# Kernel optimization log

Hardware: AMD Instinct MI355X
Metric: run time of the kernel (lower is better)

## Reference

```python
import jax, jax.numpy as jnp
import numpy as np

N_HEAD, D_EMB, D_MLP, D_HEAD = 12, 768, 3072, 64
LN_EPS = 1e-5


def setup_inputs() -> dict:
    key = jax.random.key(0)
    ks = jax.random.split(key, 12)
    s = 0.02
    return {
        "x": jax.random.normal(ks[0], (2, 4096, D_EMB), dtype=jnp.float32),
        "ln1_g": jnp.ones((D_EMB,), jnp.float32),
        "ln1_b": jnp.zeros((D_EMB,), jnp.float32),
        "wqkv_w": jax.random.normal(ks[1], (D_EMB, 3 * D_EMB), jnp.float32) * s,
        "wo_w": jax.random.normal(ks[2], (D_EMB, D_EMB), jnp.float32) * s,
        "wo_b": jnp.zeros((D_EMB,), jnp.float32),
        "ln2_g": jnp.ones((D_EMB,), jnp.float32),
        "ln2_b": jnp.zeros((D_EMB,), jnp.float32),
        "w1_w": jax.random.normal(ks[3], (D_EMB, D_MLP), jnp.float32) * s,
        "w1_b": jnp.zeros((D_MLP,), jnp.float32),
        "w2_w": jax.random.normal(ks[4], (D_MLP, D_EMB), jnp.float32) * s,
        "w2_b": jnp.zeros((D_EMB,), jnp.float32),
    }


def _layernorm(x, g, b):
    mu = jnp.mean(x, axis=-1, keepdims=True)
    var = jnp.var(x, axis=-1, keepdims=True)
    return (x - mu) * jax.lax.rsqrt(var + LN_EPS) * g + b


def _attn(x, wqkv_w, wo_w, wo_b):
    B, T, d = x.shape
    qkv = x @ wqkv_w  # [B,T,3d]
    q, k, v = jnp.split(qkv, 3, axis=-1)
    q = q.reshape(B, T, N_HEAD, D_HEAD).transpose(0, 2, 1, 3)  # [B,H,T,dh]
    k = k.reshape(B, T, N_HEAD, D_HEAD).transpose(0, 2, 1, 3)
    v = v.reshape(B, T, N_HEAD, D_HEAD).transpose(0, 2, 1, 3)
    A = jnp.einsum('bhqd,bhkd->bhqk', q, k) / np.sqrt(D_HEAD).astype(np.float32)
    mask = jnp.tril(jnp.ones((T, T), dtype=bool))
    A = jnp.where(mask, A, -jnp.inf)
    A = jax.nn.softmax(A - jax.lax.stop_gradient(jnp.max(A, axis=-1, keepdims=True)), axis=-1)
    y = jnp.einsum('bhqk,bhkd->bhqd', A, v)  # [B,H,T,dh]
    y = y.transpose(0, 2, 1, 3).reshape(B, T, d)
    return y @ wo_w + wo_b


def _mlp(x, w1_w, w1_b, w2_w, w2_b):
    h = jax.nn.gelu(x @ w1_w + w1_b, approximate=False)
    return h @ w2_w + w2_b


def reference(x, ln1_g, ln1_b, wqkv_w, wo_w, wo_b, ln2_g, ln2_b, w1_w, w1_b, w2_w, w2_b):
    x = x + _attn(_layernorm(x, ln1_g, ln1_b), wqkv_w, wo_w, wo_b)
    x = x + _mlp(_layernorm(x, ln2_g, ln2_b), w1_w, w1_b, w2_w, w2_b)
    return x
```

## Files before the change

### kernel.cpp

```cpp
#include <hip/hip_runtime.h>

#define T_SEQ 4096
#define D_EMB 768
#define N_HEAD 12
#define D_HEAD 64
#define D_MLP 3072
#define NTOK 8192
#define QSCALE 0.18033688011112043f

typedef __bf16 v8bf __attribute__((ext_vector_type(8)));
typedef float v4f __attribute__((ext_vector_type(4)));

template <int N> struct IC { static constexpr int value = N; };

__device__ __forceinline__ unsigned short f2bf(float f) {
    unsigned int u = __float_as_uint(f);
    unsigned int r = (u + 0x7fffu + ((u >> 16) & 1u)) >> 16;
    return (unsigned short)r;
}

__device__ __forceinline__ void g2lds16(const void* g, void* l) {
    __builtin_amdgcn_global_load_lds(
        (const __attribute__((address_space(1))) void*)g,
        (__attribute__((address_space(3))) void*)l, 16, 0, 0);
}

__device__ __forceinline__ int sg(int r) { return (r ^ (r >> 2)) & 3; }

__global__ void tcast_kernel(const float* __restrict__ in, unsigned short* __restrict__ out,
                             int K, int N) {
    __shared__ float tile[32][33];
    int k0 = blockIdx.y * 32, n0 = blockIdx.x * 32;
    int tx = threadIdx.x, ty = threadIdx.y;
    for (int i = ty; i < 32; i += 8)
        tile[i][tx] = in[(size_t)(k0 + i) * N + n0 + tx];
    __syncthreads();
    for (int i = ty; i < 32; i += 8)
        out[(size_t)(n0 + i) * K + k0 + tx] = f2bf(tile[tx][i]);
}

__global__ void vtrans_kernel(const unsigned short* __restrict__ in,
                              unsigned short* __restrict__ out) {
    __shared__ unsigned short tile[32][33];
    size_t base = (size_t)blockIdx.z * T_SEQ * D_HEAD;
    int t0 = blockIdx.x * 32, d0 = blockIdx.y * 32;
    int tx = threadIdx.x, ty = threadIdx.y;
    for (int i = ty; i < 32; i += 8)
        tile[i][tx] = in[base + (size_t)(t0 + i) * D_HEAD + d0 + tx];
    __syncthreads();
    size_t tbase = base + (size_t)(t0 >> 6) * 4096 + (t0 & 32);
    for (int i = ty; i < 32; i += 8)
        out[tbase + (size_t)(d0 + i) * 64 + tx] = tile[tx][i];
}

__global__ __launch_bounds__(256) void ln_kernel(const float* __restrict__ x,
                                                 const float* __restrict__ g,
                                                 const float* __restrict__ bta,
                                                 unsigned short* __restrict__ out) {
    int row = blockIdx.x;
    const float* xr = x + (size_t)row * D_EMB;
    int tid = threadIdx.x;
    float v[3];
    float s = 0.f, s2 = 0.f;
#pragma unroll
    for (int i = 0; i < 3; i++) {
        v[i] = xr[tid + i * 256];
        s += v[i];
        s2 += v[i] * v[i];
    }
#pragma unroll
    for (int o = 1; o < 64; o <<= 1) {
        s += __shfl_xor(s, o);
        s2 += __shfl_xor(s2, o);
    }
    __shared__ float red[8];
    int wave = tid >> 6, lane = tid & 63;
    if (lane == 0) { red[wave] = s; red[wave + 4] = s2; }
    __syncthreads();
    s = red[0] + red[1] + red[2] + red[3];
    s2 = red[4] + red[5] + red[6] + red[7];
    float mu = s * (1.f / 768.f);
    float var = s2 * (1.f / 768.f) - mu * mu;
    float rstd = rsqrtf(var + 1e-5f);
#pragma unroll
    for (int i = 0; i < 3; i++) {
        int c = tid + i * 256;
        out[(size_t)row * D_EMB + c] = f2bf((v[i] - mu) * rstd * g[c] + bta[c]);
    }
}

template <int EPI, int MT>
__global__ __launch_bounds__(256) void gemm_kernel(
    const unsigned short* __restrict__ A, const unsigned short* __restrict__ Bt, int K,
    int Nt, const float* __restrict__ bias, const float* __restrict__ resid,
    float* __restrict__ outF, unsigned short* __restrict__ outB,
    unsigned short* __restrict__ Qb, unsigned short* __restrict__ Kb,
    unsigned short* __restrict__ Vb) {
    constexpr int NAI = (MT == 128) ? 4 : 2;
    __shared__ unsigned short As[2][MT * 32];
    __shared__ unsigned short Bs[2][4096];
    const int tid = threadIdx.x;
    const int wave = tid >> 6, lane = tid & 63;
    const int n16 = lane & 15, kq = lane >> 4;
    const int moff = (wave >> 1) * (MT / 2), noff = (wave & 1) * 64;
    const int id = blockIdx.x;
    const int xcd = id & 7, s = id >> 3;
    const int mt = xcd * (NTOK / MT / 8) + s / Nt, nt_ = s % Nt;
    const long m0 = (long)mt * MT, nb0 = (long)nt_ * 128;

    const int c0 = (wave * 2 + 0) * 64 + lane;
    const int c1 = (wave * 2 + 1) * 64 + lane;
    const int r0 = c0 >> 2, r1 = c1 >> 2;
    const unsigned short* bP0 = Bt + (nb0 + r0) * K + (((c0 & 3) ^ sg(r0)) << 3);
    const unsigned short* bP1 = Bt + (nb0 + r1) * K + (((c1 & 3) ^ sg(r1)) << 3);
    const int ca = (MT == 128) ? c0 : (wave * 64 + lane);
    const int ra = ca >> 2;
    const unsigned short* aP0 = A + (m0 + ra) * K + (((ca & 3) ^ sg(ra)) << 3);
    const unsigned short* aP1 = (MT == 128)
        ? A + (m0 + r1) * K + (((c1 & 3) ^ sg(r1)) << 3) : nullptr;
    const int sn = sg(n16);
    const int fw = (noff + n16) * 32 + ((kq ^ sn) << 3);
    const int fa = (moff + n16) * 32 + ((kq ^ sn) << 3);

    const v4f vzero = {0.f, 0.f, 0.f, 0.f};
    v4f acc[4][NAI];
#pragma unroll
    for (int wi = 0; wi < 4; wi++)
#pragma unroll
        for (int ai = 0; ai < NAI; ai++) acc[wi][ai] = vzero;

    auto stage = [&](auto BUFC, int kpos) {
        constexpr int nb = decltype(BUFC)::value;
        if (MT == 128) {
            g2lds16(aP0 + kpos, &As[nb][(wave * 2 + 0) * 512]);
            g2lds16(aP1 + kpos, &As[nb][(wave * 2 + 1) * 512]);
        } else {
            g2lds16(aP0 + kpos, &As[nb][wave * 512]);
        }
        g2lds16(bP0 + kpos, &Bs[nb][(wave * 2 + 0) * 512]);
        g2lds16(bP1 + kpos, &Bs[nb][(wave * 2 + 1) * 512]);
    };
    auto gstep = [&](auto BUFC, int kpos, bool pref) {
        constexpr int buf = decltype(BUFC)::value;
        __syncthreads();
        if (pref) stage(IC<buf ^ 1>{}, kpos + 32);
        v8bf wf[4], af[NAI];
#pragma unroll
        for (int i = 0; i < 4; i++) wf[i] = *(const v8bf*)(&Bs[buf][fw + i * 512]);
#pragma unroll
        for (int i = 0; i < NAI; i++) af[i] = *(const v8bf*)(&As[buf][fa + i * 512]);
#pragma unroll
        for (int wi = 0; wi < 4; wi++)
#pragma unroll
            for (int ai = 0; ai < NAI; ai++)
                acc[wi][ai] = __builtin_amdgcn_mfma_f32_16x16x32_bf16(wf[wi], af[ai],
                                                                     acc[wi][ai], 0, 0, 0);
    };

    stage(IC<0>{}, 0);
#pragma unroll 1
    for (int k0 = 0; k0 < K; k0 += 64) {
        gstep(IC<0>{}, k0, true);
        gstep(IC<1>{}, k0 + 32, k0 + 64 < K);
    }

#pragma unroll
    for (int wi = 0; wi < 4; wi++) {
#pragma unroll
        for (int ai = 0; ai < NAI; ai++) {
            const long Nb = nb0 + noff + wi * 16 + kq * 4;
            const long M = m0 + moff + ai * 16 + n16;
            if (EPI == 0) {
                int which = (int)(Nb / 768);
                int c = (int)(Nb - which * 768);
                int hh = c >> 6, ii = c & 63;
                int bb = (int)(M >> 12), t = (int)(M & 4095);
                size_t dst = (((size_t)bb * N_HEAD + hh) * T_SEQ + t) * D_HEAD + ii;
                union { uint2 u2; unsigned short us[4]; } pk;
#pragma unroll
                for (int r = 0; r < 4; r++) {
                    float v = acc[wi][ai][r];
                    if (which == 0) v *= QSCALE;
                    pk.us[r] = f2bf(v);
                }
                if (which == 0) *(uint2*)(&Qb[dst]) = pk.u2;
                else if (which == 1) *(uint2*)(&Kb[dst]) = pk.u2;
                else *(uint2*)(&Vb[dst]) = pk.u2;
            } else if (EPI == 1) {
                float4 b4 = *(const float4*)(&bias[Nb]);
                float4 r4 = *(const float4*)(&resid[M * 768 + Nb]);
                float4 o4;
                o4.x = acc[wi][ai][0] + b4.x + r4.x;
                o4.y = acc[wi][ai][1] + b4.y + r4.y;
                o4.z = acc[wi][ai][2] + b4.z + r4.z;
                o4.w = acc[wi][ai][3] + b4.w + r4.w;
                *(float4*)(&outF[M * 768 + Nb]) = o4;
            } else {
                float4 b4 = *(const float4*)(&bias[Nb]);
                union { uint2 u2; unsigned short us[4]; } pk;
#pragma unroll
                for (int r = 0; r < 4; r++) {
                    float t = acc[wi][ai][r] + ((const float*)&b4)[r];
                    pk.us[r] = f2bf(0.5f * t * (1.f + erff(t * 0.70710678118f)));
                }
                *(uint2*)(&outB[M * 3072 + Nb]) = pk.u2;
            }
        }
    }
}

#define PSTR 72
__global__ __launch_bounds__(256) void attn_kernel(const unsigned short* __restrict__ Q,
                                                   const unsigned short* __restrict__ Kg,
                                                   const unsigned short* __restrict__ Vt,
                                                   unsigned short* __restrict__ y) {
    __shared__ unsigned short Kt[2][4096];
    __shared__ unsigned short Vl[2][4096];
    __shared__ unsigned short Ps[4 * 16 * PSTR];
    const int tid = threadIdx.x;
    const int wave = tid >> 6, lane = tid & 63;
    const int n16 = lane & 15, kq = lane >> 4;
    const int id = blockIdx.x;
    const int xcd = id & 7, slot = id >> 3;
    const int combo = xcd * 3 + (slot >> 5);
    const int pair = slot & 31;
    const int h = combo % N_HEAD, b = combo / N_HEAD;
    const size_t hoff = (((size_t)b * N_HEAD + h) * T_SEQ) * D_HEAD;
    const unsigned short* Qh = Q + hoff;
    const unsigned short* Kh = Kg + hoff;
    const unsigned short* Vh = Vt + hoff;
    const v4f vzero = {0.f, 0.f, 0.f, 0.f};

    const int sC0 = (wave * 2 + 0) * 64 + lane;
    const int sC1 = (wave * 2 + 1) * 64 + lane;
    const int soff0 = (sC0 >> 3) * 64 + ((((sC0 & 7) ^ ((sC0 >> 3) & 7))) << 3);
    const int soff1 = (sC1 >> 3) * 64 + ((((sC1 & 7) ^ ((sC1 >> 3) & 7))) << 3);
    const int fb0 = n16 * 64 + ((kq ^ (n16 & 7)) << 3);
    const int fb1 = n16 * 64 + (((4 + kq) ^ (n16 & 7)) << 3);
    unsigned short* pwr = &Ps[wave * 1152 + n16 * PSTR + kq * 4];
    const unsigned short* prd = &Ps[wave * 1152 + n16 * PSTR + kq * 8];
    v8bf vone;
#pragma unroll
    for (int j = 0; j < 8; j++) ((unsigned short*)&vone)[j] = 0x3F80;

    const unsigned short* knext;
    const unsigned short* vnext;
    v4f o[4], lacc;
    int qt, qglob;
    v8bf qf[2];

    auto step = [&](auto BUFC, int kt, bool pref, bool diag) {
        constexpr int buf = decltype(BUFC)::value;
        __syncthreads();
        if (pref) {
            g2lds16(knext + soff0, &Kt[buf ^ 1][(wave * 2 + 0) * 512]);
            g2lds16(knext + soff1, &Kt[buf ^ 1][(wave * 2 + 1) * 512]);
            g2lds16(vnext + soff0, &Vl[buf ^ 1][(wave * 2 + 0) * 512]);
            g2lds16(vnext + soff1, &Vl[buf ^ 1][(wave * 2 + 1) * 512]);
            knext += 4096;
            vnext += 4096;
        }
        v4f s[4];
#pragma unroll
        for (int nt = 0; nt < 4; nt++) s[nt] = vzero;
#pragma unroll
        for (int nt = 0; nt < 4; nt++) {
            v8bf k0 = *(const v8bf*)(&Kt[buf][nt * 1024 + fb0]);
            v8bf k1 = *(const v8bf*)(&Kt[buf][nt * 1024 + fb1]);
            s[nt] = __builtin_amdgcn_mfma_f32_16x16x32_bf16(k0, qf[0], s[nt], 0, 0, 0);
            s[nt] = __builtin_amdgcn_mfma_f32_16x16x32_bf16(k1, qf[1], s[nt], 0, 0, 0);
        }
#pragma unroll
        for (int nt = 0; nt < 4; nt++) {
            union { uint2 u2; __bf16 hh[4]; } pk;
#pragma unroll
            for (int r = 0; r < 4; r++) {
                float p = __builtin_amdgcn_exp2f(s[nt][r]);
                if (diag) {
                    int key = kt * 64 + nt * 16 + kq * 4 + r;
                    if (key > qglob) p = 0.f;
                }
                pk.hh[r] = (__bf16)p;
            }
            *(uint2*)(&pwr[nt * 16]) = pk.u2;
        }
#pragma unroll
        for (int ks = 0; ks < 2; ks++) {
            v8bf pa = *(const v8bf*)(&prd[ks * 32]);
            lacc = __builtin_amdgcn_mfma_f32_16x16x32_bf16(pa, vone, lacc, 0, 0, 0);
#pragma unroll
            for (int nt = 0; nt < 4; nt++) {
                v8bf vb = *(const v8bf*)(&Vl[buf][nt * 1024 + (ks ? fb1 : fb0)]);
                o[nt] = __builtin_amdgcn_mfma_f32_16x16x32_bf16(pa, vb, o[nt], 0, 0, 0);
            }
        }
    };

#pragma unroll 1
    for (int half = 0; half < 2; half++) {
        qt = half ? (63 - pair) : pair;
        qglob = qt * 64 + wave * 16 + n16;
#pragma unroll
        for (int ks = 0; ks < 2; ks++)
            qf[ks] = *(const v8bf*)(&Qh[(size_t)qglob * D_HEAD + ks * 32 + kq * 8]);
#pragma unroll
        for (int nt = 0; nt < 4; nt++) o[nt] = vzero;
        lacc = vzero;

        __syncthreads();
        g2lds16(Kh + soff0, &Kt[0][(wave * 2 + 0) * 512]);
        g2lds16(Kh + soff1, &Kt[0][(wave * 2 + 1) * 512]);
        g2lds16(Vh + soff0, &Vl[0][(wave * 2 + 0) * 512]);
        g2lds16(Vh + soff1, &Vl[0][(wave * 2 + 1) * 512]);
        knext = Kh + 4096;
        vnext = Vh + 4096;

        int kt = 0;
#pragma unroll 1
        while (kt + 2 <= qt) {
            step(IC<0>{}, kt, true, false);
            step(IC<1>{}, kt + 1, true, false);
            kt += 2;
        }
        if (kt < qt) {
            step(IC<0>{}, kt, true, false);
            step(IC<1>{}, kt + 1, false, true);
        } else {
            step(IC<0>{}, kt, false, true);
        }

        float linv[4];
#pragma unroll
        for (int r = 0; r < 4; r++) linv[r] = 1.f / lacc[r];
#pragma unroll
        for (int nt = 0; nt < 4; nt++)
#pragma unroll
            for (int r = 0; r < 4; r++) {
                int q = qt * 64 + wave * 16 + kq * 4 + r;
                float val = o[nt][r] * linv[r];
                y[((size_t)b * T_SEQ + q) * D_EMB + h * 64 + nt * 16 + n16] = f2bf(val);
            }
    }
}

extern "C" void kernel_launch(void* const* d_in, const int* in_sizes, int n_in,
                              void* d_out, int out_size, void* d_ws, size_t ws_size,
                              hipStream_t stream) {
    const float* x = (const float*)d_in[0];
    const float* ln1_g = (const float*)d_in[1];
    const float* ln1_b = (const float*)d_in[2];
    const float* wqkv_w = (const float*)d_in[3];
    const float* wo_w = (const float*)d_in[4];
    const float* wo_b = (const float*)d_in[5];
    const float* ln2_g = (const float*)d_in[6];
    const float* ln2_b = (const float*)d_in[7];
    const float* w1_w = (const float*)d_in[8];
    const float* w1_b = (const float*)d_in[9];
    const float* w2_w = (const float*)d_in[10];
    const float* w2_b = (const float*)d_in[11];
    float* out = (float*)d_out;

    char* ws = (char*)d_ws;
    size_t off = 0;
    auto alloc = [&](size_t bytes) -> void* {
        void* p = ws + off;
        off += (bytes + 255) & ~(size_t)255;
        return p;
    };
    unsigned short* xn = (unsigned short*)alloc((size_t)NTOK * D_EMB * 2);
    unsigned short* wqkvT = (unsigned short*)alloc((size_t)2304 * 768 * 2);
    unsigned short* woT = (unsigned short*)alloc((size_t)768 * 768 * 2);
    unsigned short* w1T = (unsigned short*)alloc((size_t)3072 * 768 * 2);
    unsigned short* w2T = (unsigned short*)alloc((size_t)768 * 3072 * 2);
    unsigned short* Qb = (unsigned short*)alloc((size_t)NTOK * D_EMB * 2);
    unsigned short* Kb = (unsigned short*)alloc((size_t)NTOK * D_EMB * 2);
    unsigned short* Vb = (unsigned short*)alloc((size_t)NTOK * D_EMB * 2);
    unsigned short* yb = (unsigned short*)alloc((size_t)NTOK * D_EMB * 2);
    float* res1 = (float*)alloc((size_t)NTOK * D_EMB * 4);
    unsigned short* Vtb = xn;
    unsigned short* hbuf = Qb;

    dim3 tb(32, 8);
    tcast_kernel<<<dim3(2304 / 32, 768 / 32), tb, 0, stream>>>(wqkv_w, wqkvT, 768, 2304);
    tcast_kernel<<<dim3(768 / 32, 768 / 32), tb, 0, stream>>>(wo_w, woT, 768, 768);
    tcast_kernel<<<dim3(3072 / 32, 768 / 32), tb, 0, stream>>>(w1_w, w1T, 768, 3072);
    tcast_kernel<<<dim3(768 / 32, 3072 / 32), tb, 0, stream>>>(w2_w, w2T, 3072, 768);

    ln_kernel<<<NTOK, 256, 0, stream>>>(x, ln1_g, ln1_b, xn);

    gemm_kernel<0, 64><<<2304, 256, 0, stream>>>(
        xn, wqkvT, 768, 18, nullptr, nullptr, nullptr, nullptr, Qb, Kb, Vb);

    vtrans_kernel<<<dim3(T_SEQ / 32, 2, 2 * N_HEAD), tb, 0, stream>>>(Vb, Vtb);

    attn_kernel<<<768, 256, 0, stream>>>(Qb, Kb, Vtb, yb);

    gemm_kernel<1, 64><<<768, 256, 0, stream>>>(
        yb, woT, 768, 6, wo_b, x, res1, nullptr, nullptr, nullptr, nullptr);

    ln_kernel<<<NTOK, 256, 0, stream>>>(res1, ln2_g, ln2_b, xn);

    gemm_kernel<2, 128><<<1536, 256, 0, stream>>>(
        xn, w1T, 768, 24, w1_b, nullptr, nullptr, hbuf, nullptr, nullptr, nullptr);

    gemm_kernel<1, 64><<<768, 256, 0, stream>>>(
        hbuf, w2T, 3072, 6, w2_b, res1, out, nullptr, nullptr, nullptr, nullptr);
}
```

Baseline: 453.8 us.

## Keep attention P in registers using 16x16x16 MFMA instead of LDS round-trip

Removes the shared-memory staging buffer for the softmax probabilities P. The S accumulator layout from the QK^T MFMA is fed directly as the A operand of 16x16x16 bf16 MFMAs for the PV product and the row-sum. This eliminates LDS writes and reads plus the associated latency per tile. In exchange it issues twice as many smaller MFMAs, which have lower throughput per instruction on CDNA4, and uses narrower V loads from LDS.

```diff
diff --git a/kernel.cpp b/kernel.cpp
--- a/kernel.cpp
+++ b/kernel.cpp
@@ -10,6 +10,7 @@
 
 typedef __bf16 v8bf __attribute__((ext_vector_type(8)));
 typedef float v4f __attribute__((ext_vector_type(4)));
+typedef short v4s __attribute__((ext_vector_type(4)));
 
 template <int N> struct IC { static constexpr int value = N; };
 
@@ -23,6 +24,19 @@
     __builtin_amdgcn_global_load_lds(
         (const __attribute__((address_space(1))) void*)g,
         (__attribute__((address_space(3))) void*)l, 16, 0, 0);
+}
+
+__device__ __forceinline__ v4f mfma16(v4s a, v4s b, v4f c) {
+#if __has_builtin(__builtin_amdgcn_mfma_f32_16x16x16bf16_1k)
+    return __builtin_amdgcn_mfma_f32_16x16x16bf16_1k(a, b, c, 0, 0, 0);
+#else
+    union { v4s s4; unsigned long long u; } ua, ub;
+    ua.s4 = a; ub.s4 = b;
+    union { unsigned long long u[2]; v8bf v; } pa, pb;
+    pa.u[0] = ua.u; pa.u[1] = 0ull;
+    pb.u[0] = ub.u; pb.u[1] = 0ull;
+    return __builtin_amdgcn_mfma_f32_16x16x32_bf16(pa.v, pb.v, c, 0, 0, 0);
+#endif
 }
 
 __device__ __forceinline__ int sg(int r) { return (r ^ (r >> 2)) & 3; }
@@ -209,14 +223,12 @@
     }
 }
 
-#define PSTR 72
 __global__ __launch_bounds__(256) void attn_kernel(const unsigned short* __restrict__ Q,
                                                    const unsigned short* __restrict__ Kg,
                                                    const unsigned short* __restrict__ Vt,
                                                    unsigned short* __restrict__ y) {
     __shared__ unsigned short Kt[2][4096];
     __shared__ unsigned short Vl[2][4096];
-    __shared__ unsigned short Ps[4 * 16 * PSTR];
     const int tid = threadIdx.x;
     const int wave = tid >> 6, lane = tid & 63;
     const int n16 = lane & 15, kq = lane >> 4;
@@ -237,11 +249,11 @@
     const int soff1 = (sC1 >> 3) * 64 + ((((sC1 & 7) ^ ((sC1 >> 3) & 7))) << 3);
     const int fb0 = n16 * 64 + ((kq ^ (n16 & 7)) << 3);
     const int fb1 = n16 * 64 + (((4 + kq) ^ (n16 & 7)) << 3);
-    unsigned short* pwr = &Ps[wave * 1152 + n16 * PSTR + kq * 4];
-    const unsigned short* prd = &Ps[wave * 1152 + n16 * PSTR + kq * 8];
-    v8bf vone;
-#pragma unroll
-    for (int j = 0; j < 8; j++) ((unsigned short*)&vone)[j] = 0x3F80;
+    const int vmask = n16 & 7, vkhi = kq >> 1;
+    const int vbase = n16 * 64 + (kq & 1) * 4;
+    v4s vone4;
+#pragma unroll
+    for (int j = 0; j < 4; j++) ((unsigned short*)&vone4)[j] = 0x3F80;
 
     const unsigned short* knext;
     const unsigned short* vnext;
@@ -270,28 +282,31 @@
             s[nt] = __builtin_amdgcn_mfma_f32_16x16x32_bf16(k0, qf[0], s[nt], 0, 0, 0);
             s[nt] = __builtin_amdgcn_mfma_f32_16x16x32_bf16(k1, qf[1], s[nt], 0, 0, 0);
         }
-#pragma unroll
-        for (int nt = 0; nt < 4; nt++) {
-            union { uint2 u2; __bf16 hh[4]; } pk;
+        v4s pa[4];
+#pragma unroll
+        for (int ntk = 0; ntk < 4; ntk++) {
+            union { v4s s4; __bf16 h[4]; } pk;
 #pragma unroll
             for (int r = 0; r < 4; r++) {
-                float p = __builtin_amdgcn_exp2f(s[nt][r]);
+                float p = __builtin_amdgcn_exp2f(s[ntk][r]);
                 if (diag) {
-                    int key = kt * 64 + nt * 16 + kq * 4 + r;
+                    int key = kt * 64 + ntk * 16 + kq * 4 + r;
                     if (key > qglob) p = 0.f;
                 }
-                pk.hh[r] = (__bf16)p;
+                pk.h[r] = (__bf16)p;
             }
-            *(uint2*)(&pwr[nt * 16]) = pk.u2;
-        }
-#pragma unroll
-        for (int ks = 0; ks < 2; ks++) {
-            v8bf pa = *(const v8bf*)(&prd[ks * 32]);
-            lacc = __builtin_amdgcn_mfma_f32_16x16x32_bf16(pa, vone, lacc, 0, 0, 0);
-#pragma unroll
-            for (int nt = 0; nt < 4; nt++) {
-                v8bf vb = *(const v8bf*)(&Vl[buf][nt * 1024 + (ks ? fb1 : fb0)]);
-                o[nt] = __builtin_amdgcn_mfma_f32_16x16x32_bf16(pa, vb, o[nt], 0, 0, 0);
+            pa[ntk] = pk.s4;
+        }
+#pragma unroll
+        for (int ntk = 0; ntk < 4; ntk++)
+            lacc = mfma16(pa[ntk], vone4, lacc);
+#pragma unroll
+        for (int ntd = 0; ntd < 4; ntd++) {
+#pragma unroll
+            for (int ntk = 0; ntk < 4; ntk++) {
+                v4s vb = *(const v4s*)(&Vl[buf][ntd * 1024 + vbase +
+                                               (((2 * ntk + vkhi) ^ vmask) << 3)]);
+                o[ntd] = mfma16(pa[ntk], vb, o[ntd]);
             }
         }
     };
```

Result: no change. 460.3 us (+1.4%).
